# Performance work log

Measured on AMD Instinct MI355X. Metric: run time of the kernel, lower is better.

The kernel has to match this reference:

```python
import jax, jax.numpy as jnp
import numpy as np

D_MODEL = 1024
N_HEADS = 16
HEAD_DIM = D_MODEL // N_HEADS
ROPE_BASE = 100000.0
B, NT, LD = 2, 16, 128


def setup_inputs() -> dict:
    key = jax.random.key(0)
    ks = jax.random.split(key, 10)
    s = 1.0 / np.sqrt(D_MODEL)
    inp = {
        "x": jax.random.normal(ks[0], (B, NT, LD, D_MODEL), dtype=jnp.float32),
        "datetimes": jnp.sort(jax.random.randint(ks[1], (NT,), 0, 1000, dtype=jnp.int64)
                              if jax.config.jax_enable_x64 else
                              jax.random.randint(ks[1], (NT,), 0, 1000).astype(jnp.int32)),
        "Wq": jax.random.uniform(ks[2], (D_MODEL, D_MODEL), jnp.float32, -s, s),
        "bq": jnp.zeros((D_MODEL,), jnp.float32),
        "Wk": jax.random.uniform(ks[3], (D_MODEL, D_MODEL), jnp.float32, -s, s),
        "bk": jnp.zeros((D_MODEL,), jnp.float32),
        "Wv": jax.random.uniform(ks[4], (D_MODEL, D_MODEL), jnp.float32, -s, s),
        "bv": jnp.zeros((D_MODEL,), jnp.float32),
        "Wo": jax.random.uniform(ks[5], (D_MODEL, D_MODEL), jnp.float32, -s, s),
        "bo": jnp.zeros((D_MODEL,), jnp.float32),
    }
    return inp


def _rope_cos_sin(datetimes, Ld):
    # inv_freq: (head_dim/2,)
    inv_freq = 1.0 / (ROPE_BASE ** (jnp.arange(0, HEAD_DIM, 2, dtype=jnp.float32) / HEAD_DIM))
    t = datetimes.astype(jnp.float32)              # (nt,)
    freqs = jnp.outer(t, inv_freq)                 # (nt, hd/2)
    freqs = jnp.concatenate([freqs, freqs], -1)    # (nt, hd)
    freqs = jnp.repeat(freqs, Ld, axis=0)          # (nt*Ld, hd) -- each timestep expanded over Ld spatial tokens
    cos = jnp.cos(freqs)[None, None]               # (1,1,L,hd)
    sin = jnp.sin(freqs)[None, None]
    return cos, sin


def _rotate_half(v):
    h = v.shape[-1] // 2
    return jnp.concatenate([-v[..., h:], v[..., :h]], axis=-1)


def reference(x, datetimes, Wq, bq, Wk, bk, Wv, bv, Wo, bo):
    B_, nt, Ld, D = x.shape
    L = nt * Ld
    xf = x.reshape(B_, L, D)
    # projections (torch Linear: y = x @ W.T + b)
    q = (xf @ Wq.T + bq).reshape(B_, L, N_HEADS, HEAD_DIM).transpose(0, 2, 1, 3)
    k = (xf @ Wk.T + bk).reshape(B_, L, N_HEADS, HEAD_DIM).transpose(0, 2, 1, 3)
    v = (xf @ Wv.T + bv).reshape(B_, L, N_HEADS, HEAD_DIM).transpose(0, 2, 1, 3)
    cos, sin = _rope_cos_sin(datetimes, Ld)
    q = q * cos + _rotate_half(q) * sin
    k = k * cos + _rotate_half(k) * sin
    # SDPA, no mask, not causal
    scale = 1.0 / jnp.sqrt(jnp.asarray(HEAD_DIM, x.dtype))
    scores = jnp.einsum("bhqd,bhkd->bhqk", q, k) * scale
    attn = jax.nn.softmax(scores, axis=-1)
    out = jnp.einsum("bhqk,bhkd->bhqd", attn, v)
    out = out.transpose(0, 2, 1, 3).reshape(B_, nt, Ld, D)
    out = out @ Wo.T + bo
    return out, k, v
```

## Files before the change

kernel.cpp:

```cpp
#include <hip/hip_runtime.h>

typedef short bf8 __attribute__((ext_vector_type(8)));
typedef short s4v __attribute__((ext_vector_type(4)));
typedef float f4  __attribute__((ext_vector_type(4)));


__device__ __forceinline__ short f2b(float f) {
    unsigned u = __float_as_uint(f);
    u += 0x7FFFu + ((u >> 16) & 1u);
    return (short)(u >> 16);
}

__device__ __forceinline__ f4 mfma16(bf8 a, bf8 b, f4 c) {
    return __builtin_amdgcn_mfma_f32_16x16x32_bf16(a, b, c, 0, 0, 0);
}

__device__ __forceinline__ void gl_lds16(const short* g, short* l) {
    __builtin_amdgcn_global_load_lds(
        (const __attribute__((address_space(1))) void*)g,
        (__attribute__((address_space(3))) void*)l, 16, 0, 0);
}

#define EXP2F(x) __builtin_amdgcn_exp2f(x)

__global__ __launch_bounds__(256) void conv_k(
    const float* __restrict__ x, const float* __restrict__ wq,
    const float* __restrict__ wk, const float* __restrict__ wv,
    const float* __restrict__ wo, const int* __restrict__ dt,
    short* __restrict__ xb, short* __restrict__ wqb, short* __restrict__ wkb,
    short* __restrict__ wvb, short* __restrict__ wob,
    float* __restrict__ ctab, float* __restrict__ stab) {
    if (blockIdx.x == 8192) {
        const int tid = threadIdx.x;
        const int ii = tid & 31;
        const float invf = exp2f(-(float)ii * (16.609640474436812f / 32.f));
        for (int t = tid >> 5; t < 16; t += 8) {
            const float a = (float)dt[t] * invf;
            ctab[t * 32 + ii] = cosf(a);
            stab[t * 32 + ii] = sinf(a);
        }
        return;
    }
    int idx = (blockIdx.x * 256 + threadIdx.x) * 4;
    const float* s; short* d; int off = idx;
    if (idx < 4194304)      { s = x;  d = xb; }
    else if (idx < 5242880) { s = wq; d = wqb; off = idx - 4194304; }
    else if (idx < 6291456) { s = wk; d = wkb; off = idx - 5242880; }
    else if (idx < 7340032) { s = wv; d = wvb; off = idx - 6291456; }
    else                    { s = wo; d = wob; off = idx - 7340032; }
    const float4 v = *(const float4*)&s[off];
    s4v o;
    o[0] = f2b(v.x); o[1] = f2b(v.y); o[2] = f2b(v.z); o[3] = f2b(v.w);
    *(s4v*)&d[off] = o;
}

__global__ __launch_bounds__(256) void gemm_qkv_k(
    const short* __restrict__ A, const short* __restrict__ W,
    const float* __restrict__ bq, const float* __restrict__ bk, const float* __restrict__ bv,
    float* __restrict__ out_k, float* __restrict__ out_v,
    short* __restrict__ qrot, short* __restrict__ kbb, short* __restrict__ vpk,
    const float* __restrict__ ctab, const float* __restrict__ stab) {
    __shared__ __align__(16) short As[128 * 32];
    __shared__ __align__(16) short Bs[128 * 32];

    const int n0f = blockIdx.x * 128;
    const int m0 = blockIdx.y * 128;
    const int tid = threadIdx.x;
    const int lane = tid & 63;
    const int w = tid >> 6;
    const int wr = w >> 1, wc = w & 1;
    const int g = lane >> 4, cc = lane & 15;

    const int c0 = w * 128 + lane;
    const int ar0 = c0 >> 2, ap0 = (c0 & 3) * 8;
    const short* Ag0 = A + (m0 + ar0) * 1024 + ap0;
    const short* Ag1 = Ag0 + 16 * 1024;
    const short* Wg0 = W + (n0f + ar0) * 1024 + ap0;
    const short* Wg1 = Wg0 + 16 * 1024;
    short* lA0 = &As[w * 1024];
    short* lA1 = &As[w * 1024 + 512];
    short* lB0 = &Bs[w * 1024];
    short* lB1 = &Bs[w * 1024 + 512];

    f4 acc[4][4];
#pragma unroll
    for (int i = 0; i < 4; ++i)
#pragma unroll
        for (int j = 0; j < 4; ++j) acc[i][j] = (f4){0.f, 0.f, 0.f, 0.f};

    for (int k0 = 0; k0 < 1024; k0 += 32) {
        gl_lds16(Ag0 + k0, lA0);
        gl_lds16(Ag1 + k0, lA1);
        gl_lds16(Wg0 + k0, lB0);
        gl_lds16(Wg1 + k0, lB1);
        __syncthreads();
        bf8 af[4], bfr[4];
#pragma unroll
        for (int fm = 0; fm < 4; ++fm)
            af[fm] = *(const bf8*)&As[(64 * wr + 16 * fm + cc) * 32 + 8 * g];
#pragma unroll
        for (int fn = 0; fn < 4; ++fn)
            bfr[fn] = *(const bf8*)&Bs[(64 * wc + 16 * fn + cc) * 32 + 8 * g];
#pragma unroll
        for (int fm = 0; fm < 4; ++fm)
#pragma unroll
            for (int fn = 0; fn < 4; ++fn)
                acc[fm][fn] = mfma16(af[fm], bfr[fn], acc[fm][fn]);
        __syncthreads();
    }

    const int third = n0f >> 10;
    const int n0 = n0f & 1023;
    const int h = (n0 + 64 * wc) >> 6;
    const float* bias = (third == 0) ? bq : ((third == 1) ? bk : bv);

#pragma unroll
    for (int fm = 0; fm < 4; ++fm) {
#pragma unroll
        for (int r = 0; r < 4; ++r) {
            const int m = m0 + 64 * wr + 16 * fm + 4 * g + r;
            const int b_ = m >> 11, l = m & 2047;
            const int bh2 = b_ * 16 + h;
            if (third == 2) {
                const int st2 = l >> 5, s = l & 31;
                const int j = 4 * (s >> 4) + (s & 3);
                const int g2 = (s >> 2) & 3;
#pragma unroll
                for (int fn = 0; fn < 4; ++fn) {
                    const int d = 16 * fn + cc;
                    const int n = n0 + 64 * wc + 16 * fn + cc;
                    const float val = acc[fm][fn][r] + bias[n];
                    out_v[(bh2 * 2048 + l) * 64 + d] = val;
                    const int vp = (((bh2 * 64 + st2) * 4 + g2) * 4 + (d >> 4)) * 128 + (d & 15) * 8 + j;
                    vpk[vp] = f2b(val);
                }
            } else {
                const int tt = l >> 7;
#pragma unroll
                for (int fn = 0; fn < 2; ++fn) {
                    const int d1 = 16 * fn + cc;
                    const int n1 = n0 + 64 * wc + d1;
                    const float v1 = acc[fm][fn][r] + bias[n1];
                    const float v2 = acc[fm][fn + 2][r] + bias[n1 + 32];
                    const float ct = ctab[tt * 32 + d1];
                    const float sn = stab[tt * 32 + d1];
                    const float r1 = v1 * ct - v2 * sn;
                    const float r2 = v2 * ct + v1 * sn;
                    const int oi = (bh2 * 2048 + l) * 64 + d1;
                    if (third == 0) {
                        qrot[oi]      = f2b(r1 * 0.18033688011f);
                        qrot[oi + 32] = f2b(r2 * 0.18033688011f);
                    } else {
                        out_k[oi] = r1; out_k[oi + 32] = r2;
                        const int kr = l & 31, tl = l >> 5;
                        const int kb_ = bh2 * 131072 + tl * 2048;
                        kbb[kb_ + (((kr * 128 + d1 * 2) ^ ((kr & 7) << 4)) >> 1)] = f2b(r1);
                        kbb[kb_ + (((kr * 128 + (d1 + 32) * 2) ^ ((kr & 7) << 4)) >> 1)] = f2b(r2);
                    }
                }
            }
        }
    }
}

__global__ __launch_bounds__(256) void gemm_o_k(
    const short* __restrict__ A, const short* __restrict__ W,
    const float* __restrict__ bias, float* __restrict__ out) {
    __shared__ __align__(16) short As[128 * 32];
    __shared__ __align__(16) short Bs[64 * 32];

    const int n0 = blockIdx.x * 64;
    const int m0 = blockIdx.y * 128;
    const int tid = threadIdx.x;
    const int lane = tid & 63;
    const int w = tid >> 6;
    const int wr = w >> 1, wc = w & 1;
    const int g = lane >> 4, cc = lane & 15;

    const int c0 = w * 128 + lane;
    const int ar0 = c0 >> 2, ap0 = (c0 & 3) * 8;
    const short* Ag0 = A + (m0 + ar0) * 1024 + ap0;
    const short* Ag1 = Ag0 + 16 * 1024;
    const int cb = w * 64 + lane;
    const short* Wg0 = W + (n0 + (cb >> 2)) * 1024 + (cb & 3) * 8;
    short* lA0 = &As[w * 1024];
    short* lA1 = &As[w * 1024 + 512];
    short* lB0 = &Bs[w * 512];

    f4 acc[4][2];
#pragma unroll
    for (int i = 0; i < 4; ++i) { acc[i][0] = (f4){0,0,0,0}; acc[i][1] = (f4){0,0,0,0}; }

    for (int k0 = 0; k0 < 1024; k0 += 32) {
        gl_lds16(Ag0 + k0, lA0);
        gl_lds16(Ag1 + k0, lA1);
        gl_lds16(Wg0 + k0, lB0);
        __syncthreads();
        bf8 af[4], bfr[2];
#pragma unroll
        for (int fm = 0; fm < 4; ++fm)
            af[fm] = *(const bf8*)&As[(64 * wr + 16 * fm + cc) * 32 + 8 * g];
#pragma unroll
        for (int fn = 0; fn < 2; ++fn)
            bfr[fn] = *(const bf8*)&Bs[(32 * wc + 16 * fn + cc) * 32 + 8 * g];
#pragma unroll
        for (int fm = 0; fm < 4; ++fm)
#pragma unroll
            for (int fn = 0; fn < 2; ++fn)
                acc[fm][fn] = mfma16(af[fm], bfr[fn], acc[fm][fn]);
        __syncthreads();
    }
#pragma unroll
    for (int fm = 0; fm < 4; ++fm)
#pragma unroll
        for (int r = 0; r < 4; ++r) {
            const int m = m0 + 64 * wr + 16 * fm + 4 * g + r;
#pragma unroll
            for (int fn = 0; fn < 2; ++fn) {
                const int n = n0 + 32 * wc + 16 * fn + cc;
                out[m * 1024 + n] = acc[fm][fn][r] + bias[n];
            }
        }
}

__global__ __launch_bounds__(512, 2) void attn_k(
    const short* __restrict__ q_rot, const short* __restrict__ k_b,
    const short* __restrict__ v_pk, short* __restrict__ atb) {
    __shared__ __align__(16) short lds[8192];

    const int i = blockIdx.x;
    const int xcd = i & 7, slot = i >> 3;
    const int bh = xcd + 8 * (slot & 3);
    const int qc = slot >> 2;
    const int tid = threadIdx.x;
    const int lane = tid & 63;
    const int w = tid >> 6;
    const int g = lane >> 4, cc = lane & 15;
    const int b_ = bh >> 4, h = bh & 15;
    const int q0w = qc * 256 + w * 32;

    const short* qp = q_rot + (bh * 2048 + q0w) * 64;
    const bf8 qf00 = *(const bf8*)&qp[cc * 64 + 8 * g];
    const bf8 qf01 = *(const bf8*)&qp[cc * 64 + 32 + 8 * g];
    const bf8 qf10 = *(const bf8*)&qp[(16 + cc) * 64 + 8 * g];
    const bf8 qf11 = *(const bf8*)&qp[(16 + cc) * 64 + 32 + 8 * g];

    const int part = w >> 2, sub = w & 3;
    const short* gsrc = (part ? v_pk : k_b) + bh * 131072 + sub * 512 + lane * 8;
    const int lofs = part * 2048 + sub * 512;

    const int swz = (cc & 7) << 4;
    const int koA0 = (cc * 128 + g * 16) ^ swz;
    const int koA1 = (cc * 128 + 64 + g * 16) ^ swz;
    const int koB0 = ((16 + cc) * 128 + g * 16) ^ swz;
    const int koB1 = ((16 + cc) * 128 + 64 + g * 16) ^ swz;
    const int vo = 4096 + g * 1024 + cc * 16;

    f4 O0[4], O1[4], Os0, Os1;
#pragma unroll
    for (int nb = 0; nb < 4; ++nb) { O0[nb] = (f4){0,0,0,0}; O1[nb] = (f4){0,0,0,0}; }
    Os0 = (f4){0,0,0,0}; Os1 = (f4){0,0,0,0};
    float m0 = -INFINITY, m1 = -INFINITY;

    bf8 ONES;
#pragma unroll
    for (int j = 0; j < 8; ++j) ONES[j] = (short)0x3F80;

    gl_lds16(gsrc, lds + lofs);
    asm volatile("s_waitcnt vmcnt(0)" ::: "memory");
    __builtin_amdgcn_s_barrier();

    int cur = 0;
    for (int t = 0; t < 64; ++t) {
        if (t < 63)
            gl_lds16(gsrc + (t + 1) * 2048, lds + ((cur ^ 1) * 4096 + lofs));
        const char* buf = (const char*)lds + cur * 8192;

        const bf8 ka0 = *(const bf8*)(buf + koA0);
        const bf8 ka1 = *(const bf8*)(buf + koA1);
        const bf8 kb0 = *(const bf8*)(buf + koB0);
        const bf8 kb1 = *(const bf8*)(buf + koB1);
        const bf8 vv0 = *(const bf8*)(buf + vo);
        const bf8 vv1 = *(const bf8*)(buf + vo + 256);
        const bf8 vv2 = *(const bf8*)(buf + vo + 512);
        const bf8 vv3 = *(const bf8*)(buf + vo + 768);

        __builtin_amdgcn_s_setprio(1);
        f4 sA0 = (f4){0,0,0,0}, sB0 = (f4){0,0,0,0};
        f4 sA1 = (f4){0,0,0,0}, sB1 = (f4){0,0,0,0};
        sA0 = mfma16(ka0, qf00, sA0); sA0 = mfma16(ka1, qf01, sA0);
        sB0 = mfma16(kb0, qf00, sB0); sB0 = mfma16(kb1, qf01, sB0);
        sA1 = mfma16(ka0, qf10, sA1); sA1 = mfma16(ka1, qf11, sA1);
        sB1 = mfma16(kb0, qf10, sB1); sB1 = mfma16(kb1, qf11, sB1);
        __builtin_amdgcn_s_setprio(0);

        const float t0 = fmaxf(fmaxf(fmaxf(sA0[0], sA0[1]), fmaxf(sA0[2], sA0[3])),
                               fmaxf(fmaxf(sB0[0], sB0[1]), fmaxf(sB0[2], sB0[3])));
        const float t1 = fmaxf(fmaxf(fmaxf(sA1[0], sA1[1]), fmaxf(sA1[2], sA1[3])),
                               fmaxf(fmaxf(sB1[0], sB1[1]), fmaxf(sB1[2], sB1[3])));
        if (!__all(t0 <= m0 + 8.f && t1 <= m1 + 8.f)) {
            float x0 = fmaxf(t0, __shfl_xor(t0, 16)); x0 = fmaxf(x0, __shfl_xor(x0, 32));
            float x1 = fmaxf(t1, __shfl_xor(t1, 16)); x1 = fmaxf(x1, __shfl_xor(x1, 32));
            const float n0 = fmaxf(m0, x0), n1 = fmaxf(m1, x1);
            const float c0 = EXP2F(m0 - n0), c1 = EXP2F(m1 - n1);
#pragma unroll
            for (int r = 0; r < 4; ++r) {
                const float cr0 = __shfl(c0, 4 * g + r);
                const float cr1 = __shfl(c1, 4 * g + r);
                O0[0][r] *= cr0; O0[1][r] *= cr0; O0[2][r] *= cr0; O0[3][r] *= cr0;
                Os0[r] *= cr0;
                O1[0][r] *= cr1; O1[1][r] *= cr1; O1[2][r] *= cr1; O1[3][r] *= cr1;
                Os1[r] *= cr1;
            }
            m0 = n0; m1 = n1;
        }

        union { bf8 v; unsigned u[4]; } P0, P1;
        {
            float p[8];
#pragma unroll
            for (int r = 0; r < 4; ++r) { p[r] = EXP2F(sA0[r] - m0); p[4 + r] = EXP2F(sB0[r] - m0); }
#pragma unroll
            for (int k2 = 0; k2 < 4; ++k2)
                P0.u[k2] = (__float_as_uint(p[2 * k2]) >> 16) |
                           (__float_as_uint(p[2 * k2 + 1]) & 0xFFFF0000u);
        }
        {
            float p[8];
#pragma unroll
            for (int r = 0; r < 4; ++r) { p[r] = EXP2F(sA1[r] - m1); p[4 + r] = EXP2F(sB1[r] - m1); }
#pragma unroll
            for (int k2 = 0; k2 < 4; ++k2)
                P1.u[k2] = (__float_as_uint(p[2 * k2]) >> 16) |
                           (__float_as_uint(p[2 * k2 + 1]) & 0xFFFF0000u);
        }

        __builtin_amdgcn_s_setprio(1);
        O0[0] = mfma16(P0.v, vv0, O0[0]); O0[1] = mfma16(P0.v, vv1, O0[1]);
        O0[2] = mfma16(P0.v, vv2, O0[2]); O0[3] = mfma16(P0.v, vv3, O0[3]);
        Os0 = mfma16(P0.v, ONES, Os0);
        O1[0] = mfma16(P1.v, vv0, O1[0]); O1[1] = mfma16(P1.v, vv1, O1[1]);
        O1[2] = mfma16(P1.v, vv2, O1[2]); O1[3] = mfma16(P1.v, vv3, O1[3]);
        Os1 = mfma16(P1.v, ONES, Os1);
        __builtin_amdgcn_s_setprio(0);

        asm volatile("s_waitcnt vmcnt(0)" ::: "memory");
        __builtin_amdgcn_s_barrier();
        cur ^= 1;
    }

    short* ob = atb + (b_ * 2048 + q0w) * 1024 + h * 64 + cc;
#pragma unroll
    for (int r = 0; r < 4; ++r) {
        const float i0 = 1.f / Os0[r];
        const float i1 = 1.f / Os1[r];
#pragma unroll
        for (int nb = 0; nb < 4; ++nb) {
            ob[(4 * g + r) * 1024 + nb * 16]        = f2b(O0[nb][r] * i0);
            ob[(16 + 4 * g + r) * 1024 + nb * 16]   = f2b(O1[nb][r] * i1);
        }
    }
}

extern "C" void kernel_launch(void* const* d_in, const int* in_sizes, int n_in,
                              void* d_out, int out_size, void* d_ws, size_t ws_size,
                              hipStream_t stream) {
    const float* x  = (const float*)d_in[0];
    const int*   dt = (const int*)d_in[1];
    const float* Wq = (const float*)d_in[2];
    const float* bq = (const float*)d_in[3];
    const float* Wk = (const float*)d_in[4];
    const float* bk = (const float*)d_in[5];
    const float* Wv = (const float*)d_in[6];
    const float* bv = (const float*)d_in[7];
    const float* Wo = (const float*)d_in[8];
    const float* bo = (const float*)d_in[9];

    float* out   = (float*)d_out;
    float* out_k = out + 4194304;
    float* out_v = out + 8388608;

    short* xb   = (short*)d_ws;
    short* wqb  = xb + 4194304;
    short* wkb  = wqb + 1048576;
    short* wvb  = wkb + 1048576;
    short* wob  = wvb + 1048576;
    short* qrot = wob + 1048576;
    short* kbb  = qrot + 4194304;
    short* vpk  = kbb + 4194304;
    short* atb  = vpk + 4194304;
    float* ctab = (float*)(atb + 4194304);
    float* stab = ctab + 512;

    conv_k<<<8193, 256, 0, stream>>>(x, Wq, Wk, Wv, Wo, dt,
                                     xb, wqb, wkb, wvb, wob, ctab, stab);
    gemm_qkv_k<<<dim3(24, 32), 256, 0, stream>>>(xb, wqb, bq, bk, bv,
                                                 out_k, out_v, qrot, kbb, vpk, ctab, stab);
    attn_k<<<256, 512, 0, stream>>>(qrot, kbb, vpk, atb);
    gemm_o_k<<<dim3(16, 32), 256, 0, stream>>>(atb, wob, bo, out);
}
```

Before: 208.6 us.

## Double-buffer GEMM LDS loads and triple-buffer K/V in a finer-grained attention

Both projection GEMMs now double-buffer their LDS tiles. The next K-slice is loaded asynchronously while MFMAs run on the current one, and the MFMA section is wrapped in raised wave priority. The attention kernel cuts each wave to 16 query rows instead of 32 and doubles the grid to 512 blocks, with a higher occupancy hint. It also switches K/V staging to a three-stage ring with prefetch distance two. The aim is to hide global-load latency and raise occupancy, at the cost of more LDS and twice the K/V LDS reads per query.

```diff
diff --git a/kernel.cpp b/kernel.cpp
--- a/kernel.cpp
+++ b/kernel.cpp
@@ -60,8 +60,8 @@
     float* __restrict__ out_k, float* __restrict__ out_v,
     short* __restrict__ qrot, short* __restrict__ kbb, short* __restrict__ vpk,
     const float* __restrict__ ctab, const float* __restrict__ stab) {
-    __shared__ __align__(16) short As[128 * 32];
-    __shared__ __align__(16) short Bs[128 * 32];
+    __shared__ __align__(16) short As[2 * 4096];
+    __shared__ __align__(16) short Bs[2 * 4096];
 
     const int n0f = blockIdx.x * 128;
     const int m0 = blockIdx.y * 128;
@@ -77,10 +77,7 @@
     const short* Ag1 = Ag0 + 16 * 1024;
     const short* Wg0 = W + (n0f + ar0) * 1024 + ap0;
     const short* Wg1 = Wg0 + 16 * 1024;
-    short* lA0 = &As[w * 1024];
-    short* lA1 = &As[w * 1024 + 512];
-    short* lB0 = &Bs[w * 1024];
-    short* lB1 = &Bs[w * 1024 + 512];
+    const int sof = w * 1024;
 
     f4 acc[4][4];
 #pragma unroll
@@ -88,24 +85,36 @@
 #pragma unroll
         for (int j = 0; j < 4; ++j) acc[i][j] = (f4){0.f, 0.f, 0.f, 0.f};
 
-    for (int k0 = 0; k0 < 1024; k0 += 32) {
-        gl_lds16(Ag0 + k0, lA0);
-        gl_lds16(Ag1 + k0, lA1);
-        gl_lds16(Wg0 + k0, lB0);
-        gl_lds16(Wg1 + k0, lB1);
-        __syncthreads();
+    gl_lds16(Ag0, &As[sof]);
+    gl_lds16(Ag1, &As[sof + 512]);
+    gl_lds16(Wg0, &Bs[sof]);
+    gl_lds16(Wg1, &Bs[sof + 512]);
+    __syncthreads();
+
+    for (int t = 0; t < 32; ++t) {
+        if (t < 31) {
+            const int nb = ((t + 1) & 1) * 4096;
+            const int kk = (t + 1) * 32;
+            gl_lds16(Ag0 + kk, &As[nb + sof]);
+            gl_lds16(Ag1 + kk, &As[nb + sof + 512]);
+            gl_lds16(Wg0 + kk, &Bs[nb + sof]);
+            gl_lds16(Wg1 + kk, &Bs[nb + sof + 512]);
+        }
+        const int cb = (t & 1) * 4096;
         bf8 af[4], bfr[4];
 #pragma unroll
         for (int fm = 0; fm < 4; ++fm)
-            af[fm] = *(const bf8*)&As[(64 * wr + 16 * fm + cc) * 32 + 8 * g];
+            af[fm] = *(const bf8*)&As[cb + (64 * wr + 16 * fm + cc) * 32 + 8 * g];
 #pragma unroll
         for (int fn = 0; fn < 4; ++fn)
-            bfr[fn] = *(const bf8*)&Bs[(64 * wc + 16 * fn + cc) * 32 + 8 * g];
+            bfr[fn] = *(const bf8*)&Bs[cb + (64 * wc + 16 * fn + cc) * 32 + 8 * g];
+        __builtin_amdgcn_s_setprio(1);
 #pragma unroll
         for (int fm = 0; fm < 4; ++fm)
 #pragma unroll
             for (int fn = 0; fn < 4; ++fn)
                 acc[fm][fn] = mfma16(af[fm], bfr[fn], acc[fm][fn]);
+        __builtin_amdgcn_s_setprio(0);
         __syncthreads();
     }
 
@@ -166,8 +175,8 @@
 __global__ __launch_bounds__(256) void gemm_o_k(
     const short* __restrict__ A, const short* __restrict__ W,
     const float* __restrict__ bias, float* __restrict__ out) {
-    __shared__ __align__(16) short As[128 * 32];
-    __shared__ __align__(16) short Bs[64 * 32];
+    __shared__ __align__(16) short As[2 * 4096];
+    __shared__ __align__(16) short Bs[2 * 2048];
 
     const int n0 = blockIdx.x * 64;
     const int m0 = blockIdx.y * 128;
@@ -181,33 +190,42 @@
     const int ar0 = c0 >> 2, ap0 = (c0 & 3) * 8;
     const short* Ag0 = A + (m0 + ar0) * 1024 + ap0;
     const short* Ag1 = Ag0 + 16 * 1024;
-    const int cb = w * 64 + lane;
-    const short* Wg0 = W + (n0 + (cb >> 2)) * 1024 + (cb & 3) * 8;
-    short* lA0 = &As[w * 1024];
-    short* lA1 = &As[w * 1024 + 512];
-    short* lB0 = &Bs[w * 512];
+    const int cb0 = w * 64 + lane;
+    const short* Wg0 = W + (n0 + (cb0 >> 2)) * 1024 + (cb0 & 3) * 8;
+    const int sofA = w * 1024, sofB = w * 512;
 
     f4 acc[4][2];
 #pragma unroll
     for (int i = 0; i < 4; ++i) { acc[i][0] = (f4){0,0,0,0}; acc[i][1] = (f4){0,0,0,0}; }
 
-    for (int k0 = 0; k0 < 1024; k0 += 32) {
-        gl_lds16(Ag0 + k0, lA0);
-        gl_lds16(Ag1 + k0, lA1);
-        gl_lds16(Wg0 + k0, lB0);
-        __syncthreads();
+    gl_lds16(Ag0, &As[sofA]);
+    gl_lds16(Ag1, &As[sofA + 512]);
+    gl_lds16(Wg0, &Bs[sofB]);
+    __syncthreads();
+
+    for (int t = 0; t < 32; ++t) {
+        if (t < 31) {
+            const int kk = (t + 1) * 32;
+            const int nbA = ((t + 1) & 1) * 4096, nbB = ((t + 1) & 1) * 2048;
+            gl_lds16(Ag0 + kk, &As[nbA + sofA]);
+            gl_lds16(Ag1 + kk, &As[nbA + sofA + 512]);
+            gl_lds16(Wg0 + kk, &Bs[nbB + sofB]);
+        }
+        const int ca = (t & 1) * 4096, cbs = (t & 1) * 2048;
         bf8 af[4], bfr[2];
 #pragma unroll
         for (int fm = 0; fm < 4; ++fm)
-            af[fm] = *(const bf8*)&As[(64 * wr + 16 * fm + cc) * 32 + 8 * g];
+            af[fm] = *(const bf8*)&As[ca + (64 * wr + 16 * fm + cc) * 32 + 8 * g];
 #pragma unroll
         for (int fn = 0; fn < 2; ++fn)
-            bfr[fn] = *(const bf8*)&Bs[(32 * wc + 16 * fn + cc) * 32 + 8 * g];
+            bfr[fn] = *(const bf8*)&Bs[cbs + (32 * wc + 16 * fn + cc) * 32 + 8 * g];
+        __builtin_amdgcn_s_setprio(1);
 #pragma unroll
         for (int fm = 0; fm < 4; ++fm)
 #pragma unroll
             for (int fn = 0; fn < 2; ++fn)
                 acc[fm][fn] = mfma16(af[fm], bfr[fn], acc[fm][fn]);
+        __builtin_amdgcn_s_setprio(0);
         __syncthreads();
     }
 #pragma unroll
@@ -223,10 +241,10 @@
         }
 }
 
-__global__ __launch_bounds__(512, 2) void attn_k(
+__global__ __launch_bounds__(512, 4) void attn_k(
     const short* __restrict__ q_rot, const short* __restrict__ k_b,
     const short* __restrict__ v_pk, short* __restrict__ atb) {
-    __shared__ __align__(16) short lds[8192];
+    __shared__ __align__(16) short lds[12288];
 
     const int i = blockIdx.x;
     const int xcd = i & 7, slot = i >> 3;
@@ -237,13 +255,11 @@
     const int w = tid >> 6;
     const int g = lane >> 4, cc = lane & 15;
     const int b_ = bh >> 4, h = bh & 15;
-    const int q0w = qc * 256 + w * 32;
+    const int q0w = qc * 128 + w * 16;
 
     const short* qp = q_rot + (bh * 2048 + q0w) * 64;
-    const bf8 qf00 = *(const bf8*)&qp[cc * 64 + 8 * g];
-    const bf8 qf01 = *(const bf8*)&qp[cc * 64 + 32 + 8 * g];
-    const bf8 qf10 = *(const bf8*)&qp[(16 + cc) * 64 + 8 * g];
-    const bf8 qf11 = *(const bf8*)&qp[(16 + cc) * 64 + 32 + 8 * g];
+    const bf8 qf0 = *(const bf8*)&qp[cc * 64 + 8 * g];
+    const bf8 qf1 = *(const bf8*)&qp[cc * 64 + 32 + 8 * g];
 
     const int part = w >> 2, sub = w & 3;
     const short* gsrc = (part ? v_pk : k_b) + bh * 131072 + sub * 512 + lane * 8;
@@ -256,24 +272,27 @@
     const int koB1 = ((16 + cc) * 128 + 64 + g * 16) ^ swz;
     const int vo = 4096 + g * 1024 + cc * 16;
 
-    f4 O0[4], O1[4], Os0, Os1;
-#pragma unroll
-    for (int nb = 0; nb < 4; ++nb) { O0[nb] = (f4){0,0,0,0}; O1[nb] = (f4){0,0,0,0}; }
-    Os0 = (f4){0,0,0,0}; Os1 = (f4){0,0,0,0};
-    float m0 = -INFINITY, m1 = -INFINITY;
+    f4 O[4], Os;
+#pragma unroll
+    for (int nb = 0; nb < 4; ++nb) O[nb] = (f4){0, 0, 0, 0};
+    Os = (f4){0, 0, 0, 0};
+    float m = -INFINITY;
 
     bf8 ONES;
 #pragma unroll
     for (int j = 0; j < 8; ++j) ONES[j] = (short)0x3F80;
 
     gl_lds16(gsrc, lds + lofs);
-    asm volatile("s_waitcnt vmcnt(0)" ::: "memory");
+    gl_lds16(gsrc + 2048, lds + 4096 + lofs);
+    asm volatile("s_waitcnt vmcnt(1)" ::: "memory");
     __builtin_amdgcn_s_barrier();
 
     int cur = 0;
     for (int t = 0; t < 64; ++t) {
-        if (t < 63)
-            gl_lds16(gsrc + (t + 1) * 2048, lds + ((cur ^ 1) * 4096 + lofs));
+        if (t < 62) {
+            int stg = cur + 2; if (stg >= 3) stg -= 3;
+            gl_lds16(gsrc + (t + 2) * 2048, lds + stg * 4096 + lofs);
+        }
         const char* buf = (const char*)lds + cur * 8192;
 
         const bf8 ka0 = *(const bf8*)(buf + koA0);
@@ -286,79 +305,57 @@
         const bf8 vv3 = *(const bf8*)(buf + vo + 768);
 
         __builtin_amdgcn_s_setprio(1);
-        f4 sA0 = (f4){0,0,0,0}, sB0 = (f4){0,0,0,0};
-        f4 sA1 = (f4){0,0,0,0}, sB1 = (f4){0,0,0,0};
-        sA0 = mfma16(ka0, qf00, sA0); sA0 = mfma16(ka1, qf01, sA0);
-        sB0 = mfma16(kb0, qf00, sB0); sB0 = mfma16(kb1, qf01, sB0);
-        sA1 = mfma16(ka0, qf10, sA1); sA1 = mfma16(ka1, qf11, sA1);
-        sB1 = mfma16(kb0, qf10, sB1); sB1 = mfma16(kb1, qf11, sB1);
+        f4 sA = (f4){0, 0, 0, 0}, sB = (f4){0, 0, 0, 0};
+        sA = mfma16(ka0, qf0, sA); sA = mfma16(ka1, qf1, sA);
+        sB = mfma16(kb0, qf0, sB); sB = mfma16(kb1, qf1, sB);
         __builtin_amdgcn_s_setprio(0);
 
-        const float t0 = fmaxf(fmaxf(fmaxf(sA0[0], sA0[1]), fmaxf(sA0[2], sA0[3])),
-                               fmaxf(fmaxf(sB0[0], sB0[1]), fmaxf(sB0[2], sB0[3])));
-        const float t1 = fmaxf(fmaxf(fmaxf(sA1[0], sA1[1]), fmaxf(sA1[2], sA1[3])),
-                               fmaxf(fmaxf(sB1[0], sB1[1]), fmaxf(sB1[2], sB1[3])));
-        if (!__all(t0 <= m0 + 8.f && t1 <= m1 + 8.f)) {
-            float x0 = fmaxf(t0, __shfl_xor(t0, 16)); x0 = fmaxf(x0, __shfl_xor(x0, 32));
-            float x1 = fmaxf(t1, __shfl_xor(t1, 16)); x1 = fmaxf(x1, __shfl_xor(x1, 32));
-            const float n0 = fmaxf(m0, x0), n1 = fmaxf(m1, x1);
-            const float c0 = EXP2F(m0 - n0), c1 = EXP2F(m1 - n1);
+        const float t0 = fmaxf(fmaxf(fmaxf(sA[0], sA[1]), fmaxf(sA[2], sA[3])),
+                               fmaxf(fmaxf(sB[0], sB[1]), fmaxf(sB[2], sB[3])));
+        if (!__all(t0 <= m + 8.f)) {
+            float x0 = fmaxf(t0, __shfl_xor(t0, 16));
+            x0 = fmaxf(x0, __shfl_xor(x0, 32));
+            const float mn = fmaxf(m, x0);
+            const float c0 = EXP2F(m - mn);
 #pragma unroll
             for (int r = 0; r < 4; ++r) {
-                const float cr0 = __shfl(c0, 4 * g + r);
-                const float cr1 = __shfl(c1, 4 * g + r);
-                O0[0][r] *= cr0; O0[1][r] *= cr0; O0[2][r] *= cr0; O0[3][r] *= cr0;
-                Os0[r] *= cr0;
-                O1[0][r] *= cr1; O1[1][r] *= cr1; O1[2][r] *= cr1; O1[3][r] *= cr1;
-                Os1[r] *= cr1;
+                const float cr = __shfl(c0, 4 * g + r);
+                O[0][r] *= cr; O[1][r] *= cr; O[2][r] *= cr; O[3][r] *= cr;
+                Os[r] *= cr;
             }
-            m0 = n0; m1 = n1;
-        }
-
-        union { bf8 v; unsigned u[4]; } P0, P1;
+            m = mn;
+        }
+
+        union { bf8 v; unsigned u[4]; } P;
         {
             float p[8];
 #pragma unroll
-            for (int r = 0; r < 4; ++r) { p[r] = EXP2F(sA0[r] - m0); p[4 + r] = EXP2F(sB0[r] - m0); }
+            for (int r = 0; r < 4; ++r) { p[r] = EXP2F(sA[r] - m); p[4 + r] = EXP2F(sB[r] - m); }
 #pragma unroll
             for (int k2 = 0; k2 < 4; ++k2)
-                P0.u[k2] = (__float_as_uint(p[2 * k2]) >> 16) |
-                           (__float_as_uint(p[2 * k2 + 1]) & 0xFFFF0000u);
-        }
-        {
-            float p[8];
-#pragma unroll
-            for (int r = 0; r < 4; ++r) { p[r] = EXP2F(sA1[r] - m1); p[4 + r] = EXP2F(sB1[r] - m1); }
-#pragma unroll
-            for (int k2 = 0; k2 < 4; ++k2)
-                P1.u[k2] = (__float_as_uint(p[2 * k2]) >> 16) |
-                           (__float_as_uint(p[2 * k2 + 1]) & 0xFFFF0000u);
+                P.u[k2] = (__float_as_uint(p[2 * k2]) >> 16) |
+                          (__float_as_uint(p[2 * k2 + 1]) & 0xFFFF0000u);
         }
 
         __builtin_amdgcn_s_setprio(1);
-        O0[0] = mfma16(P0.v, vv0, O0[0]); O0[1] = mfma16(P0.v, vv1, O0[1]);
-        O0[2] = mfma16(P0.v, vv2, O0[2]); O0[3] = mfma16(P0.v, vv3, O0[3]);
-        Os0 = mfma16(P0.v, ONES, Os0);
-        O1[0] = mfma16(P1.v, vv0, O1[0]); O1[1] = mfma16(P1.v, vv1, O1[1]);
-        O1[2] = mfma16(P1.v, vv2, O1[2]); O1[3] = mfma16(P1.v, vv3, O1[3]);
-        Os1 = mfma16(P1.v, ONES, Os1);
+        O[0] = mfma16(P.v, vv0, O[0]); O[1] = mfma16(P.v, vv1, O[1]);
+        O[2] = mfma16(P.v, vv2, O[2]); O[3] = mfma16(P.v, vv3, O[3]);
+        Os = mfma16(P.v, ONES, Os);
         __builtin_amdgcn_s_setprio(0);
 
-        asm volatile("s_waitcnt vmcnt(0)" ::: "memory");
+        if (t < 62) { asm volatile("s_waitcnt vmcnt(1)" ::: "memory"); }
+        else        { asm volatile("s_waitcnt vmcnt(0)" ::: "memory"); }
         __builtin_amdgcn_s_barrier();
-        cur ^= 1;
+        cur = (cur == 2) ? 0 : cur + 1;
     }
 
     short* ob = atb + (b_ * 2048 + q0w) * 1024 + h * 64 + cc;
 #pragma unroll
     for (int r = 0; r < 4; ++r) {
-        const float i0 = 1.f / Os0[r];
-        const float i1 = 1.f / Os1[r];
-#pragma unroll
-        for (int nb = 0; nb < 4; ++nb) {
-            ob[(4 * g + r) * 1024 + nb * 16]        = f2b(O0[nb][r] * i0);
-            ob[(16 + 4 * g + r) * 1024 + nb * 16]   = f2b(O1[nb][r] * i1);
-        }
+        const float i0 = 1.f / Os[r];
+#pragma unroll
+        for (int nb = 0; nb < 4; ++nb)
+            ob[(4 * g + r) * 1024 + nb * 16] = f2b(O[nb][r] * i0);
     }
 }
 
@@ -396,6 +393,6 @@
                                      xb, wqb, wkb, wvb, wob, ctab, stab);
     gemm_qkv_k<<<dim3(24, 32), 256, 0, stream>>>(xb, wqb, bq, bk, bv,
                                                  out_k, out_v, qrot, kbb, vpk, ctab, stab);
-    attn_k<<<256, 512, 0, stream>>>(qrot, kbb, vpk, atb);
+    attn_k<<<512, 512, 0, stream>>>(qrot, kbb, vpk, atb);
     gemm_o_k<<<dim3(16, 32), 256, 0, stream>>>(atb, wob, bo, out);
 }
```

Result: slower. 213.6 us (+2.4%).
